# Kernel optimization log

Hardware: AMD Instinct MI355X
Metric: run time of the kernel (lower is better)

The kernel has to match this reference:

```python
import jax, jax.numpy as jnp
import numpy as np

N_NODES = 50000
N_EDGES = 600000
F_IN = 64
N_GRAPHS = 2000
OUT_DIM = 1
BN_EPS = 1e-5


def _bn(x, gamma, beta):
    # BatchNorm1d training-mode forward: biased batch stats over node/row dim
    m = jnp.mean(x, axis=0)
    v = jnp.var(x, axis=0)
    return (x - m) * jax.lax.rsqrt(v + BN_EPS) * gamma + beta


def _gcn(x, W, b, src, dst):
    # PyG GCNConv: h = x @ W; symmetric-normalized aggregation with self-loops; bias after agg
    n = x.shape[0]
    h = x @ W                                    # [N, C_out]
    ones = jnp.ones((src.shape[0],), h.dtype)
    deg = jax.ops.segment_sum(ones, dst, num_segments=n) + 1.0  # +1 self-loop
    dinv = jax.lax.rsqrt(deg)
    norm = (dinv[src] * dinv[dst])[:, None]      # [E, 1]
    agg = jax.ops.segment_sum(h[src] * norm, dst, num_segments=n)
    agg = agg + h * (1.0 / deg)[:, None]         # self-loop term: deg^{-1/2}*deg^{-1/2}
    return agg + b


def _pool_mean(x, batch, g):
    s = jax.ops.segment_sum(x, batch, num_segments=g)
    c = jax.ops.segment_sum(jnp.ones((x.shape[0],), x.dtype), batch, num_segments=g)
    return s / jnp.maximum(c, 1.0)[:, None]


def _forward(xc, xs, W1c, b1c, g1c, be1c, W2c, b2c, g2c, be2c,
             W1s, b1s, g1s, be1s, W2s, b2s, g2s, be2s,
             Wf1, bf1, gf1, bef1, Wf2, bf2,
             src_c, dst_c, src_s, dst_s, batch):
    hc = jax.nn.relu(_bn(_gcn(xc, W1c, b1c, src_c, dst_c), g1c, be1c))
    hc = jax.nn.relu(_bn(_gcn(hc, W2c, b2c, src_c, dst_c), g2c, be2c))
    hs = jax.nn.relu(_bn(_gcn(xs, W1s, b1s, src_s, dst_s), g1s, be1s))
    hs = jax.nn.relu(_bn(_gcn(hs, W2s, b2s, src_s, dst_s), g2s, be2s))
    pc = _pool_mean(hc, batch, N_GRAPHS)         # [G, 64]
    ps = _pool_mean(hs, batch, N_GRAPHS)         # [G, 64]
    h = jnp.concatenate([pc, ps], axis=1)        # [G, 128]
    h = jax.nn.relu(_bn(h @ Wf1 + bf1, gf1, bef1))  # dropout is identity in eval
    return h @ Wf2 + bf2                         # [G, OUT_DIM]


def setup_inputs() -> dict:
    key = jax.random.key(0)
    ks = jax.random.split(key, 16)

    def glorot(k, fan_in, fan_out):
        s = np.sqrt(2.0 / (fan_in + fan_out)).astype(np.float32)
        return jax.random.normal(k, (fan_in, fan_out), jnp.float32) * s

    inp = {
        'x_chromophore': jax.random.normal(ks[0], (N_NODES, F_IN), jnp.float32),
        'x_solvent': jax.random.normal(ks[1], (N_NODES, F_IN), jnp.float32),
        'edge_index_chromophore': jax.random.randint(ks[2], (2, N_EDGES), 0, N_NODES),
        'edge_index_solvent': jax.random.randint(ks[3], (2, N_EDGES), 0, N_NODES),
        'batch': jnp.sort(jax.random.randint(ks[4], (N_NODES,), 0, N_GRAPHS)),
        # chromophore branch params
        'W1c': glorot(ks[5], F_IN, 128), 'b1c': jnp.zeros((128,), jnp.float32),
        'g1c': jnp.ones((128,), jnp.float32), 'be1c': jnp.zeros((128,), jnp.float32),
        'W2c': glorot(ks[6], 128, 64), 'b2c': jnp.zeros((64,), jnp.float32),
        'g2c': jnp.ones((64,), jnp.float32), 'be2c': jnp.zeros((64,), jnp.float32),
        # solvent branch params
        'W1s': glorot(ks[7], F_IN, 128), 'b1s': jnp.zeros((128,), jnp.float32),
        'g1s': jnp.ones((128,), jnp.float32), 'be1s': jnp.zeros((128,), jnp.float32),
        'W2s': glorot(ks[8], 128, 64), 'b2s': jnp.zeros((64,), jnp.float32),
        'g2s': jnp.ones((64,), jnp.float32), 'be2s': jnp.zeros((64,), jnp.float32),
        # MLP head
        'Wf1': glorot(ks[9], 128, 64), 'bf1': jnp.zeros((64,), jnp.float32),
        'gf1': jnp.ones((64,), jnp.float32), 'bef1': jnp.zeros((64,), jnp.float32),
        'Wf2': glorot(ks[10], 64, OUT_DIM), 'bf2': jnp.zeros((OUT_DIM,), jnp.float32),
    }
    return inp


def reference(x_chromophore, x_solvent, edge_index_chromophore, edge_index_solvent, batch,
              W1c, b1c, g1c, be1c, W2c, b2c, g2c, be2c,
              W1s, b1s, g1s, be1s, W2s, b2s, g2s, be2s,
              Wf1, bf1, gf1, bef1, Wf2, bf2):
    src_c, dst_c = edge_index_chromophore[0], edge_index_chromophore[1]
    src_s, dst_s = edge_index_solvent[0], edge_index_solvent[1]
    return _forward(x_chromophore, x_solvent,
                    W1c, b1c, g1c, be1c, W2c, b2c, g2c, be2c,
                    W1s, b1s, g1s, be1s, W2s, b2s, g2s, be2s,
                    Wf1, bf1, gf1, bef1, Wf2, bf2,
                    src_c, dst_c, src_s, dst_s, batch)
```

## Files before the change

kernel.cpp:

```cpp
#include <hip/hip_runtime.h>
#include <hip/hip_bf16.h>
#include <cstdint>
#include <cstddef>

#define NN 50000
#define NE 600000
#define NG 2000
#define NBUCK 49
#define SLOTS 16
#define NCHUNK 3125

typedef __attribute__((ext_vector_type(8))) short bf8;
typedef __attribute__((ext_vector_type(4))) float f32x4;

__device__ __forceinline__ unsigned short f2bf(float f) {
    uint32_t u = __float_as_uint(f);
    uint32_t r = (u + 0x7FFFu + ((u >> 16) & 1u)) >> 16;
    return (unsigned short)r;
}
__device__ __forceinline__ float bf2f(unsigned short h) {
    return __uint_as_float(((uint32_t)h) << 16);
}
__device__ __forceinline__ float lo16(uint32_t v) { return __uint_as_float(v << 16); }
__device__ __forceinline__ float hi16(uint32_t v) { return __uint_as_float(v & 0xFFFF0000u); }

__global__ __launch_bounds__(256) void conv_bf16_kernel(const float* __restrict__ x0,
                                                        const float* __restrict__ x1,
                                                        unsigned short* __restrict__ out) {
    int b = blockIdx.y;
    const float* x = b ? x1 : x0;
    unsigned short* o = out + (size_t)b * NN * 64;
    int i = (blockIdx.x * 256 + threadIdx.x) * 4;
    if (i + 3 < NN * 64) {
        float4 v = *(const float4*)&x[i];
        ushort4 r = make_ushort4(f2bf(v.x), f2bf(v.y), f2bf(v.z), f2bf(v.w));
        *(ushort4*)&o[i] = r;
    }
}

template<int K, int N>
__global__ __launch_bounds__(256) void pack_w(const float* __restrict__ W0,
                                              const float* __restrict__ W1,
                                              unsigned short* __restrict__ out) {
    int b = blockIdx.y;
    const float* W = b ? W1 : W0;
    unsigned short* o = out + (size_t)b * K * N;
    int idx = blockIdx.x * 256 + threadIdx.x;
    const int total = (N / 16) * (K / 32) * 64;
    if (idx >= total) return;
    int l = idx & 63;
    int th = idx >> 6;
    int h = th % (K / 32);
    int t = th / (K / 32);
    int col = t * 16 + (l & 15);
    int k0 = h * 32 + (l >> 4) * 8;
    ushort4 lo = make_ushort4(f2bf(W[(k0 + 0) * N + col]), f2bf(W[(k0 + 1) * N + col]),
                              f2bf(W[(k0 + 2) * N + col]), f2bf(W[(k0 + 3) * N + col]));
    ushort4 hi = make_ushort4(f2bf(W[(k0 + 4) * N + col]), f2bf(W[(k0 + 5) * N + col]),
                              f2bf(W[(k0 + 6) * N + col]), f2bf(W[(k0 + 7) * N + col]));
    *(ushort4*)&o[idx * 8] = lo;
    *(ushort4*)&o[idx * 8 + 4] = hi;
}

__global__ __launch_bounds__(256) void bucket_hist(const int* __restrict__ d0,
                                                   const int* __restrict__ d1,
                                                   int* __restrict__ bucketCnt, int nE) {
    int b = blockIdx.y;
    const int* dst = b ? d1 : d0;
    __shared__ int h[NBUCK];
    for (int i = threadIdx.x; i < NBUCK; i += 256) h[i] = 0;
    __syncthreads();
    for (int e = blockIdx.x * 256 + threadIdx.x; e < nE; e += gridDim.x * 256)
        atomicAdd(&h[dst[e] >> 10], 1);
    __syncthreads();
    for (int i = threadIdx.x; i < NBUCK; i += 256)
        if (h[i]) atomicAdd(&bucketCnt[b * NBUCK + i], h[i]);
}

__global__ void bucket_scan(const int* __restrict__ bucketCnt,
                            int* __restrict__ bucketOff, int* __restrict__ bucketCur) {
    int b = threadIdx.x;
    if (b < 2) {
        int run = 0;
        for (int i = 0; i < NBUCK; ++i) {
            bucketOff[b * NBUCK + i] = run;
            bucketCur[b * NBUCK + i] = run;
            run += bucketCnt[b * NBUCK + i];
        }
    }
}

__global__ __launch_bounds__(256) void bucket_scatter(const int* __restrict__ s0,
                                                      const int* __restrict__ d0,
                                                      const int* __restrict__ s1,
                                                      const int* __restrict__ d1,
                                                      int* __restrict__ bucketCur,
                                                      uint32_t* __restrict__ bent, int nE) {
    int b = blockIdx.y;
    const int* src = b ? s1 : s0;
    const int* dst = b ? d1 : d0;
    __shared__ int cnt[NBUCK];
    __shared__ int base[NBUCK];
    const int tid = threadIdx.x;
    for (int i = tid; i < NBUCK; i += 256) cnt[i] = 0;
    __syncthreads();

    const int e0 = blockIdx.x * 2048 + tid;
    int bk[8], slot[8];
    uint32_t pay[8];
#pragma unroll
    for (int k = 0; k < 8; ++k) {
        int e = e0 + k * 256;
        if (e < nE) {
            int d = dst[e], s = src[e];
            bk[k] = d >> 10;
            pay[k] = ((uint32_t)(d & 1023) << 16) | (uint32_t)s;
            slot[k] = atomicAdd(&cnt[bk[k]], 1);
        } else bk[k] = -1;
    }
    __syncthreads();
    for (int i = tid; i < NBUCK; i += 256) {
        int c = cnt[i];
        base[i] = c ? atomicAdd(&bucketCur[b * NBUCK + i], c) : 0;
    }
    __syncthreads();
#pragma unroll
    for (int k = 0; k < 8; ++k)
        if (bk[k] >= 0)
            bent[(size_t)b * NE + base[bk[k]] + slot[k]] = pay[k];
}

__global__ __launch_bounds__(256) void csr_build(const uint32_t* __restrict__ bent,
                                                 const int* __restrict__ bucketOff,
                                                 const int* __restrict__ bucketCnt,
                                                 int* __restrict__ row_ptr,
                                                 float* __restrict__ dinv,
                                                 uint16_t* __restrict__ perm) {
    __shared__ int lcnt[1024];
    __shared__ int lcur[1024];
    __shared__ int sscan[256];
    const int bk = blockIdx.x;
    const int b = blockIdx.y;
    const int tid = threadIdx.x;
    const int ebase = bucketOff[b * NBUCK + bk];
    const int ecnt = bucketCnt[b * NBUCK + bk];
    const int node0 = bk << 10;
    const uint32_t* be = bent + (size_t)b * NE + ebase;
    int* rp = row_ptr + b * (NN + 1);
    float* dv = dinv + (size_t)b * NN;
    uint16_t* pm = perm + (size_t)b * NE + ebase;

    for (int i = tid; i < 1024; i += 256) lcnt[i] = 0;
    __syncthreads();
    for (int i = tid; i < ecnt; i += 256) atomicAdd(&lcnt[be[i] >> 16], 1);
    __syncthreads();

    int c[4], s = 0;
#pragma unroll
    for (int j = 0; j < 4; ++j) { c[j] = lcnt[tid * 4 + j]; s += c[j]; }
    sscan[tid] = s;
    __syncthreads();
    for (int off = 1; off < 256; off <<= 1) {
        int v = (tid >= off) ? sscan[tid - off] : 0;
        __syncthreads();
        sscan[tid] += v;
        __syncthreads();
    }
    int run = sscan[tid] - s;
#pragma unroll
    for (int j = 0; j < 4; ++j) {
        int nl = tid * 4 + j;
        int g = node0 + nl;
        if (g < NN) {
            rp[g] = ebase + run;
            lcur[nl] = run;
            dv[g] = rsqrtf((float)c[j] + 1.0f);
        }
        run += c[j];
    }
    if (bk == NBUCK - 1 && tid == 0) rp[NN] = ebase + ecnt;
    __syncthreads();

    for (int i = tid; i < ecnt; i += 256) {
        uint32_t en = be[i];
        int nl = en >> 16;
        int pos = atomicAdd(&lcur[nl], 1);
        pm[pos] = (uint16_t)(en & 0xFFFFu);
    }
}

__global__ __launch_bounds__(256) void weight_fill(const uint16_t* __restrict__ perm,
                                                   const float* __restrict__ dinv,
                                                   uint32_t* __restrict__ permw, int nE) {
    int b = blockIdx.y;
    const uint16_t* pm = perm + (size_t)b * NE;
    const float* dv = dinv + (size_t)b * NN;
    uint32_t* pw = permw + (size_t)b * NE;
    int i = (blockIdx.x * 256 + threadIdx.x) * 4;
    if (i + 3 < nE) {
        ushort4 s4 = *(const ushort4*)&pm[i];
        uint4 o;
        o.x = ((uint32_t)f2bf(dv[s4.x]) << 16) | (uint32_t)s4.x;
        o.y = ((uint32_t)f2bf(dv[s4.y]) << 16) | (uint32_t)s4.y;
        o.z = ((uint32_t)f2bf(dv[s4.z]) << 16) | (uint32_t)s4.z;
        o.w = ((uint32_t)f2bf(dv[s4.w]) << 16) | (uint32_t)s4.w;
        *(uint4*)&pw[i] = o;
    } else {
        for (; i < nE; ++i) {
            uint16_t s = pm[i];
            pw[i] = ((uint32_t)f2bf(dv[s]) << 16) | (uint32_t)s;
        }
    }
}

__global__ __launch_bounds__(256) void graph_ranges(const int* __restrict__ batch,
                                                    int* __restrict__ gstart,
                                                    int* __restrict__ gend, int n) {
    int i = blockIdx.x * 256 + threadIdx.x;
    if (i >= n) return;
    int g = batch[i];
    if (i == 0 || batch[i - 1] != g) gstart[g] = i;
    if (i == n - 1 || batch[i + 1] != g) gend[g] = i + 1;
}

__global__ __launch_bounds__(256) void gemm1_mfma(const unsigned short* __restrict__ Xbf,
                                                  const unsigned short* __restrict__ Wp,
                                                  unsigned short* __restrict__ Y) {
    const int b = blockIdx.y;
    const unsigned short* __restrict__ X = Xbf + (size_t)b * NN * 64;
    const unsigned short* __restrict__ W = Wp + (size_t)b * 64 * 128;
    unsigned short* __restrict__ Yb = Y + (size_t)b * NN * 128;
    const int tid = threadIdx.x;
    const int w = tid >> 6, lane = tid & 63;
    const int chunk = blockIdx.x * 4 + w;
    if (chunk >= NCHUNK) return;
    const int m = lane & 15, quad = lane >> 4;

    const int row = chunk * 16 + m;
    bf8 a0 = *(const bf8*)&X[(size_t)row * 64 + quad * 8];
    bf8 a1 = *(const bf8*)&X[(size_t)row * 64 + 32 + quad * 8];
    f32x4 acc[8];
#pragma unroll
    for (int t = 0; t < 8; ++t) acc[t] = (f32x4){0.f, 0.f, 0.f, 0.f};
#pragma unroll
    for (int t = 0; t < 8; ++t) {
        bf8 b0 = *(const bf8*)&W[((t * 2 + 0) * 64 + lane) * 8];
        bf8 b1 = *(const bf8*)&W[((t * 2 + 1) * 64 + lane) * 8];
        acc[t] = __builtin_amdgcn_mfma_f32_16x16x32_bf16(b0, a0, acc[t], 0, 0, 0);
        acc[t] = __builtin_amdgcn_mfma_f32_16x16x32_bf16(b1, a1, acc[t], 0, 0, 0);
    }
#pragma unroll
    for (int t = 0; t < 8; ++t) {
        uint32_t lo = (uint32_t)f2bf(acc[t][0]) | ((uint32_t)f2bf(acc[t][1]) << 16);
        uint32_t hi = (uint32_t)f2bf(acc[t][2]) | ((uint32_t)f2bf(acc[t][3]) << 16);
        *(uint2*)&Yb[(size_t)row * 128 + t * 16 + quad * 4] = make_uint2(lo, hi);
    }
}

__global__ __launch_bounds__(256) void stats128_bf16(const unsigned short* __restrict__ Y,
                                                     float* __restrict__ sums) {
    const int b = blockIdx.y;
    const unsigned short* __restrict__ Yb = Y + (size_t)b * NN * 128;
    const int g = threadIdx.x & 31;
    const int rs = threadIdx.x >> 5;
    float s0 = 0.f, s1 = 0.f, s2 = 0.f, s3 = 0.f;
    float q0 = 0.f, q1 = 0.f, q2 = 0.f, q3 = 0.f;
    for (int r = blockIdx.x * 8 + rs; r < NN; r += gridDim.x * 8) {
        uint2 v = *(const uint2*)&Yb[(size_t)r * 128 + g * 4];
        float x0 = lo16(v.x);
        float x1 = hi16(v.x);
        float x2 = lo16(v.y);
        float x3 = hi16(v.y);
        s0 += x0; s1 += x1; s2 += x2; s3 += x3;
        q0 = fmaf(x0, x0, q0); q1 = fmaf(x1, x1, q1);
        q2 = fmaf(x2, x2, q2); q3 = fmaf(x3, x3, q3);
    }
    __shared__ float ls[8][128], lq[8][128];
    *(float4*)&ls[rs][g * 4] = make_float4(s0, s1, s2, s3);
    *(float4*)&lq[rs][g * 4] = make_float4(q0, q1, q2, q3);
    __syncthreads();
    if (threadIdx.x < 128) {
        const int c = threadIdx.x;
        float S = 0.f, Q = 0.f;
#pragma unroll
        for (int k = 0; k < 8; ++k) { S += ls[k][c]; Q += lq[k][c]; }
        int slot = blockIdx.x & (SLOTS - 1);
        float* sb = sums + (size_t)(b * SLOTS + slot) * 256;
        atomicAdd(&sb[c], S);
        atomicAdd(&sb[128 + c], Q);
    }
}

__global__ __launch_bounds__(256) void gemm2_mfma(const unsigned short* __restrict__ H1,
                                                  const unsigned short* __restrict__ Wp,
                                                  const float* __restrict__ sums,
                                                  const float* __restrict__ g0,
                                                  const float* __restrict__ g1,
                                                  const float* __restrict__ be0,
                                                  const float* __restrict__ be1,
                                                  unsigned short* __restrict__ Y) {
    __shared__ float scLds[128], shLds[128];
    const int b = blockIdx.y;
    const unsigned short* __restrict__ X = H1 + (size_t)b * NN * 128;
    const unsigned short* __restrict__ W = Wp + (size_t)b * 128 * 64;
    unsigned short* __restrict__ Yb = Y + (size_t)b * NN * 64;
    const int tid = threadIdx.x;

    if (tid < 128) {
        float s = 0.f, s2 = 0.f;
#pragma unroll
        for (int k = 0; k < SLOTS; ++k) {
            const float* sb = sums + (size_t)(b * SLOTS + k) * 256;
            s += sb[tid];
            s2 += sb[128 + tid];
        }
        const float invN = 1.0f / (float)NN;
        float mean = s * invN;
        float var = s2 * invN - mean * mean;
        float gamma = b ? g1[tid] : g0[tid];
        float beta = b ? be1[tid] : be0[tid];
        float sc = gamma * rsqrtf(var + 1e-5f);
        scLds[tid] = sc;
        shLds[tid] = beta - mean * sc;
    }
    __syncthreads();

    const int w = tid >> 6, lane = tid & 63;
    const int chunk = blockIdx.x * 4 + w;
    if (chunk >= NCHUNK) return;
    const int m = lane & 15, quad = lane >> 4;
    const int row = chunk * 16 + m;

    f32x4 acc[4];
#pragma unroll
    for (int t = 0; t < 4; ++t) acc[t] = (f32x4){0.f, 0.f, 0.f, 0.f};
#pragma unroll
    for (int h = 0; h < 4; ++h) {
        const int k0 = h * 32 + quad * 8;
        bf8 araw = *(const bf8*)&X[(size_t)row * 128 + k0];
        float4 sc0 = *(const float4*)&scLds[k0];
        float4 sc1 = *(const float4*)&scLds[k0 + 4];
        float4 sh0 = *(const float4*)&shLds[k0];
        float4 sh1 = *(const float4*)&shLds[k0 + 4];
        float scv[8] = {sc0.x, sc0.y, sc0.z, sc0.w, sc1.x, sc1.y, sc1.z, sc1.w};
        float shv[8] = {sh0.x, sh0.y, sh0.z, sh0.w, sh1.x, sh1.y, sh1.z, sh1.w};
        bf8 af;
#pragma unroll
        for (int j = 0; j < 8; ++j) {
            float v = bf2f((unsigned short)araw[j]);
            v = fmaxf(fmaf(v, scv[j], shv[j]), 0.f);
            af[j] = (short)f2bf(v);
        }
#pragma unroll
        for (int t = 0; t < 4; ++t) {
            bf8 bf = *(const bf8*)&W[((t * 4 + h) * 64 + lane) * 8];
            acc[t] = __builtin_amdgcn_mfma_f32_16x16x32_bf16(bf, af, acc[t], 0, 0, 0);
        }
    }
#pragma unroll
    for (int t = 0; t < 4; ++t) {
        uint32_t lo = (uint32_t)f2bf(acc[t][0]) | ((uint32_t)f2bf(acc[t][1]) << 16);
        uint32_t hi = (uint32_t)f2bf(acc[t][2]) | ((uint32_t)f2bf(acc[t][3]) << 16);
        *(uint2*)&Yb[(size_t)row * 64 + t * 16 + quad * 4] = make_uint2(lo, hi);
    }
}

template<bool STATS>
__global__ __launch_bounds__(256) void agg2_kernel(const unsigned short* __restrict__ hall,
                                                   const int* __restrict__ row_ptr,
                                                   const uint32_t* __restrict__ permw,
                                                   const float* __restrict__ dinv,
                                                   unsigned short* __restrict__ out,
                                                   float* __restrict__ sums, int nNodes) {
    const int bid = blockIdx.x;
    const int xcd = bid & 7;
    const int b = xcd >> 2;
    const int j = (bid >> 3) * 4 + (xcd & 3);
    const unsigned short* __restrict__ h = hall + (size_t)b * NN * 64;
    const int* rp = row_ptr + b * (NN + 1);
    const uint32_t* pe = permw + (size_t)b * NE;
    const float* dv = dinv + (size_t)b * NN;
    unsigned short* ob = out + (size_t)b * nNodes * 64;

    const int w = threadIdx.x >> 6;
    const int wave = j * 4 + w;
    const int lane = threadIdx.x & 63;
    const int q = lane & 15;
    const int r = lane >> 4;
    float f0 = 0.f, f1 = 0.f, f2 = 0.f, f3 = 0.f;
    const bool active = wave < nNodes;
    if (active) {
        const int d = wave;
        const float di = dv[d];
        const int p0 = rp[d], p1 = rp[d + 1];
        float a0 = 0.f, a1 = 0.f, a2 = 0.f, a3 = 0.f;
        for (int p = p0; p < p1; p += 16) {
            uint32_t en[4];
#pragma unroll
            for (int k = 0; k < 4; ++k) {
                int e = p + k * 4 + r;
                bool vld = e < p1;
                en[k] = pe[vld ? e : p0];
                if (!vld) en[k] &= 0xFFFFu;
            }
#pragma unroll
            for (int k = 0; k < 4; ++k) {
                const int idx = (int)(en[k] & 0xFFFFu);
                const float wk = __uint_as_float(en[k] & 0xFFFF0000u);
                const uint2 hv = *(const uint2*)&h[(size_t)idx * 64 + q * 4];
                a0 = fmaf(wk, lo16(hv.x), a0);
                a1 = fmaf(wk, hi16(hv.x), a1);
                a2 = fmaf(wk, lo16(hv.y), a2);
                a3 = fmaf(wk, hi16(hv.y), a3);
            }
        }
        a0 += __shfl_xor(a0, 16, 64); a0 += __shfl_xor(a0, 32, 64);
        a1 += __shfl_xor(a1, 16, 64); a1 += __shfl_xor(a1, 32, 64);
        a2 += __shfl_xor(a2, 16, 64); a2 += __shfl_xor(a2, 32, 64);
        a3 += __shfl_xor(a3, 16, 64); a3 += __shfl_xor(a3, 32, 64);
        const uint2 sv = *(const uint2*)&h[(size_t)d * 64 + q * 4];
        f0 = di * fmaf(di, lo16(sv.x), a0);
        f1 = di * fmaf(di, hi16(sv.x), a1);
        f2 = di * fmaf(di, lo16(sv.y), a2);
        f3 = di * fmaf(di, hi16(sv.y), a3);
        if (r == 0) {
            uint32_t o0 = (uint32_t)f2bf(f0) | ((uint32_t)f2bf(f1) << 16);
            uint32_t o1 = (uint32_t)f2bf(f2) | ((uint32_t)f2bf(f3) << 16);
            *(uint2*)&ob[(size_t)d * 64 + q * 4] = make_uint2(o0, o1);
        }
    }
    if constexpr (STATS) {
        __shared__ float ls[256], ls2[256];
        if (lane < 16) {
            *(float4*)&ls[w * 64 + q * 4]  = make_float4(f0, f1, f2, f3);
            *(float4*)&ls2[w * 64 + q * 4] = make_float4(f0 * f0, f1 * f1, f2 * f2, f3 * f3);
        }
        __syncthreads();
        if (threadIdx.x < 64) {
            const int t = threadIdx.x;
            float s  = ls[t]  + ls[t + 64]  + ls[t + 128]  + ls[t + 192];
            float s2 = ls2[t] + ls2[t + 64] + ls2[t + 128] + ls2[t + 192];
            int slot = j & (SLOTS - 1);
            float* sb = sums + ((size_t)(b * SLOTS + slot) * 2) * 64;
            atomicAdd(&sb[t], s);
            atomicAdd(&sb[64 + t], s2);
        }
    }
}

__global__ __launch_bounds__(128) void pool_head_kernel(const unsigned short* __restrict__ x,
                                                        const float* __restrict__ sums,
                                                        const float* __restrict__ g0,
                                                        const float* __restrict__ g1,
                                                        const float* __restrict__ be0,
                                                        const float* __restrict__ be1,
                                                        const int* __restrict__ gstart,
                                                        const int* __restrict__ gend,
                                                        const float* __restrict__ Wf1,
                                                        float* __restrict__ T) {
    __shared__ float row[128];
    const int g = blockIdx.x;
    const int c = threadIdx.x;
    const int b = c >> 6;
    const int ch = c & 63;
    float s0 = 0.f, s20 = 0.f;
#pragma unroll
    for (int k = 0; k < SLOTS; ++k) {
        const float* sb = sums + ((size_t)(b * SLOTS + k) * 2) * 64;
        s0 += sb[ch];
        s20 += sb[64 + ch];
    }
    const float invN = 1.0f / (float)NN;
    float mean = s0 * invN;
    float var = s20 * invN - mean * mean;
    float gamma = b ? g1[ch] : g0[ch];
    float beta = b ? be1[ch] : be0[ch];
    float sc = gamma * rsqrtf(var + 1e-5f);
    float sh = beta - mean * sc;

    const unsigned short* xb = x + (size_t)b * NN * 64;
    const int start = gstart[g];
    const int end = gend[g];
    float s = 0.f;
    for (int r = start; r < end; ++r)
        s += fmaxf(fmaf(bf2f(xb[(size_t)r * 64 + ch]), sc, sh), 0.f);
    float cf = (float)(end - start);
    row[c] = s / fmaxf(cf, 1.f);
    __syncthreads();

    if (c < 64) {
        float acc = 0.f;
#pragma unroll 8
        for (int k = 0; k < 128; ++k) acc = fmaf(row[k], Wf1[k * 64 + c], acc);
        T[(size_t)g * 64 + c] = acc;
    }
}

template<int C>
__global__ __launch_bounds__(256) void bn_stats_kernel(const float* __restrict__ x, int n,
                                                       float* __restrict__ sums) {
    constexpr int RP = 256 / C;
    __shared__ float ls[256], ls2[256];
    int c = threadIdx.x % C;
    int sub = threadIdx.x / C;
    float s = 0.f, s2 = 0.f;
    for (int r = blockIdx.x * RP + sub; r < n; r += gridDim.x * RP) {
        float v = x[(size_t)r * C + c];
        s += v; s2 += v * v;
    }
    ls[threadIdx.x] = s; ls2[threadIdx.x] = s2;
    __syncthreads();
    if (sub == 0) {
#pragma unroll
        for (int k = 1; k < RP; ++k) { s += ls[k * C + c]; s2 += ls2[k * C + c]; }
        atomicAdd(&sums[c], s);
        atomicAdd(&sums[C + c], s2);
    }
}

__global__ __launch_bounds__(64) void head_final_kernel(const float* __restrict__ T,
                                                        const float* __restrict__ hsums,
                                                        const float* __restrict__ gf1,
                                                        const float* __restrict__ bef1,
                                                        const float* __restrict__ Wf2,
                                                        const float* __restrict__ bf2,
                                                        float* __restrict__ out) {
    int g = blockIdx.x;
    int c = threadIdx.x;
    const float invG = 1.0f / (float)NG;
    float mean = hsums[c] * invG;
    float var = hsums[64 + c] * invG - mean * mean;
    float sc = gf1[c] * rsqrtf(var + 1e-5f);
    float sh = bef1[c] - mean * sc;
    float v = fmaxf(fmaf(T[(size_t)g * 64 + c], sc, sh), 0.f) * Wf2[c];
#pragma unroll
    for (int off = 32; off > 0; off >>= 1) v += __shfl_down(v, off, 64);
    if (c == 0) out[g] = v + bf2[0];
}


static inline size_t alignup(size_t x) { return (x + 255) & ~(size_t)255; }

extern "C" void kernel_launch(void* const* d_in, const int* in_sizes, int n_in,
                              void* d_out, int out_size, void* d_ws, size_t ws_size,
                              hipStream_t stream) {
    const float* xc  = (const float*)d_in[0];
    const float* xs  = (const float*)d_in[1];
    const int*   eic = (const int*)d_in[2];
    const int*   eis = (const int*)d_in[3];
    const int*   batch = (const int*)d_in[4];
    const float* W1c = (const float*)d_in[5];
    const float* g1c = (const float*)d_in[7];
    const float* be1c = (const float*)d_in[8];
    const float* W2c = (const float*)d_in[9];
    const float* g2c = (const float*)d_in[11];
    const float* be2c = (const float*)d_in[12];
    const float* W1s = (const float*)d_in[13];
    const float* g1s = (const float*)d_in[15];
    const float* be1s = (const float*)d_in[16];
    const float* W2s = (const float*)d_in[17];
    const float* g2s = (const float*)d_in[19];
    const float* be2s = (const float*)d_in[20];
    const float* Wf1 = (const float*)d_in[21];
    const float* gf1 = (const float*)d_in[23];
    const float* bef1 = (const float*)d_in[24];
    const float* Wf2 = (const float*)d_in[25];
    const float* bf2 = (const float*)d_in[26];
    float* out = (float*)d_out;

    char* ws = (char*)d_ws;
    size_t off = 0;
    auto alloc = [&](size_t bytes) { char* p = ws + off; off += alignup(bytes); return p; };

    int*      bucketCnt = (int*)alloc(2 * NBUCK * 4);
    int*      bucketOff = (int*)alloc(2 * NBUCK * 4);
    int*      bucketCur = (int*)alloc(2 * NBUCK * 4);
    uint32_t* bent      = (uint32_t*)alloc((size_t)2 * NE * 4);
    uint16_t* perm      = (uint16_t*)alloc(((size_t)2 * NE + 64) * 2);
    int*      row_ptr   = (int*)alloc(2 * (NN + 1) * 4);
    float*    dinv      = (float*)alloc((size_t)2 * NN * 4);
    int*      gbound    = (int*)alloc((size_t)2 * NG * 4);
    unsigned short* xbf   = (unsigned short*)alloc((size_t)2 * NN * 64 * 2);
    unsigned short* aggbf = (unsigned short*)alloc((size_t)2 * NN * 64 * 2);
    unsigned short* h1bf  = (unsigned short*)alloc((size_t)2 * NN * 128 * 2);
    unsigned short* h2bf  = (unsigned short*)alloc((size_t)2 * NN * 64 * 2);
    unsigned short* Wp1   = (unsigned short*)alloc((size_t)2 * 64 * 128 * 2);
    unsigned short* Wp2   = (unsigned short*)alloc((size_t)2 * 128 * 64 * 2);
    float*    sums1     = (float*)alloc(((size_t)2 * SLOTS * 256 + (size_t)2 * SLOTS * 128 + 128) * 4);
    float*    sums2     = sums1 + (size_t)2 * SLOTS * 256;
    float*    hsums     = sums2 + (size_t)2 * SLOTS * 128;
    float*    T         = (float*)alloc((size_t)NG * 64 * 4);
    int*      gstart    = gbound;
    int*      gend      = gbound + NG;

    const size_t statBytes = ((size_t)2 * SLOTS * 256 + (size_t)2 * SLOTS * 128 + 128) * 4;
    const int gemmBlocks = (NCHUNK + 3) / 4;
    const int aggBlocks = 25000;

    conv_bf16_kernel<<<dim3((NN * 64 / 4 + 255) / 256, 2), 256, 0, stream>>>(xc, xs, xbf);
    pack_w<64, 128><<<dim3(4, 2), 256, 0, stream>>>(W1c, W1s, Wp1);
    pack_w<128, 64><<<dim3(4, 2), 256, 0, stream>>>(W2c, W2s, Wp2);
    hipMemsetAsync(sums1, 0, statBytes, stream);
    hipMemsetAsync(gbound, 0, 2 * NG * 4, stream);
    graph_ranges<<<(NN + 255) / 256, 256, 0, stream>>>(batch, gstart, gend, NN);

    hipMemsetAsync(bucketCnt, 0, 2 * NBUCK * 4, stream);
    bucket_hist<<<dim3(64, 2), 256, 0, stream>>>(eic + NE, eis + NE, bucketCnt, NE);
    bucket_scan<<<1, 64, 0, stream>>>(bucketCnt, bucketOff, bucketCur);
    bucket_scatter<<<dim3((NE + 2047) / 2048, 2), 256, 0, stream>>>(
        eic, eic + NE, eis, eis + NE, bucketCur, bent, NE);
    csr_build<<<dim3(NBUCK, 2), 256, 0, stream>>>(bent, bucketOff, bucketCnt,
                                                  row_ptr, dinv, perm);
    weight_fill<<<dim3((NE / 4 + 255) / 256, 2), 256, 0, stream>>>(perm, dinv, bent, NE);

    agg2_kernel<false><<<aggBlocks, 256, 0, stream>>>(
        xbf, row_ptr, bent, dinv, aggbf, nullptr, NN);
    gemm1_mfma<<<dim3(gemmBlocks, 2), 256, 0, stream>>>(aggbf, Wp1, h1bf);
    stats128_bf16<<<dim3(256, 2), 256, 0, stream>>>(h1bf, sums1);

    gemm2_mfma<<<dim3(gemmBlocks, 2), 256, 0, stream>>>(h1bf, Wp2, sums1,
                                                        g1c, g1s, be1c, be1s, h2bf);
    agg2_kernel<true><<<aggBlocks, 256, 0, stream>>>(
        h2bf, row_ptr, bent, dinv, aggbf, sums2, NN);

    pool_head_kernel<<<NG, 128, 0, stream>>>(aggbf, sums2, g2c, g2s, be2c, be2s,
                                             gstart, gend, Wf1, T);

    bn_stats_kernel<64><<<32, 256, 0, stream>>>(T, NG, hsums);
    head_final_kernel<<<NG, 64, 0, stream>>>(T, hsums, gf1, bef1, Wf2, bf2, out);
}
```

Before: 346.2 us.

## Pack per-node degree, dinv and first edges into 128-byte records for aggregation

Adds a rec_fill kernel that writes one 32-word record per node holding the edge count, dinv, the row offset and up to 28 packed edge entries. The aggregation kernel then loads the record with a single coalesced read and broadcasts the entries by shuffle, replacing separate row_ptr, dinv and edge-list loads. This removes dependent pointer-chasing latency in both aggregation passes. In exchange it adds an extra kernel and about 25 MB of record writes, and nodes with more than 28 edges still take the old loop.

```diff
diff --git a/kernel.cpp b/kernel.cpp
--- a/kernel.cpp
+++ b/kernel.cpp
@@ -9,6 +9,8 @@
 #define NBUCK 49
 #define SLOTS 16
 #define NCHUNK 3125
+#define RECW 32
+#define RECE 28
 
 typedef __attribute__((ext_vector_type(8))) short bf8;
 typedef __attribute__((ext_vector_type(4))) float f32x4;
@@ -213,6 +215,35 @@
     }
 }
 
+__global__ __launch_bounds__(256) void rec_fill(const int* __restrict__ row_ptr,
+                                                const float* __restrict__ dinv,
+                                                const uint32_t* __restrict__ permw,
+                                                uint32_t* __restrict__ recb) {
+    const int b = blockIdx.y;
+    const int tid = threadIdx.x;
+    const int node = blockIdx.x * 16 + (tid >> 4);
+    const int sub = tid & 15;
+    if (node >= NN) return;
+    const int* rp = row_ptr + b * (NN + 1);
+    const uint32_t* pe = permw + (size_t)b * NE;
+    const int p0 = rp[node], p1 = rp[node + 1];
+    const int cnt = p1 - p0;
+    const int cmin = cnt < RECE ? cnt : RECE;
+    uint2 o;
+    if (sub == 0) {
+        o.x = (uint32_t)cnt;
+        o.y = __float_as_uint(dinv[(size_t)b * NN + node]);
+    } else if (sub == 1) {
+        o.x = (uint32_t)p0;
+        o.y = 0u;
+    } else {
+        int j0 = sub * 2 - 4;
+        o.x = (j0 < cmin) ? pe[p0 + j0] : 0u;
+        o.y = (j0 + 1 < cmin) ? pe[p0 + j0 + 1] : 0u;
+    }
+    *(uint2*)&recb[((size_t)b * NN + node) * RECW + sub * 2] = o;
+}
+
 __global__ __launch_bounds__(256) void graph_ranges(const int* __restrict__ batch,
                                                     int* __restrict__ gstart,
                                                     int* __restrict__ gend, int n) {
@@ -366,10 +397,9 @@
 }
 
 template<bool STATS>
-__global__ __launch_bounds__(256) void agg2_kernel(const unsigned short* __restrict__ hall,
-                                                   const int* __restrict__ row_ptr,
+__global__ __launch_bounds__(256) void agg4_kernel(const unsigned short* __restrict__ hall,
+                                                   const uint32_t* __restrict__ recb,
                                                    const uint32_t* __restrict__ permw,
-                                                   const float* __restrict__ dinv,
                                                    unsigned short* __restrict__ out,
                                                    float* __restrict__ sums, int nNodes) {
     const int bid = blockIdx.x;
@@ -377,41 +407,57 @@
     const int b = xcd >> 2;
     const int j = (bid >> 3) * 4 + (xcd & 3);
     const unsigned short* __restrict__ h = hall + (size_t)b * NN * 64;
-    const int* rp = row_ptr + b * (NN + 1);
+    const uint32_t* __restrict__ rec = recb + (size_t)b * NN * RECW;
     const uint32_t* pe = permw + (size_t)b * NE;
-    const float* dv = dinv + (size_t)b * NN;
     unsigned short* ob = out + (size_t)b * nNodes * 64;
 
     const int w = threadIdx.x >> 6;
-    const int wave = j * 4 + w;
+    const int d = j * 4 + w;
     const int lane = threadIdx.x & 63;
     const int q = lane & 15;
     const int r = lane >> 4;
     float f0 = 0.f, f1 = 0.f, f2 = 0.f, f3 = 0.f;
-    const bool active = wave < nNodes;
+    const bool active = d < nNodes;
     if (active) {
-        const int d = wave;
-        const float di = dv[d];
-        const int p0 = rp[d], p1 = rp[d + 1];
+        const uint32_t rv = rec[(size_t)d * RECW + (lane & 31)];
+        const int cnt = (int)__shfl(rv, 0, 64);
+        const float di = __uint_as_float(__shfl(rv, 1, 64));
+        const int cmin = cnt < RECE ? cnt : RECE;
         float a0 = 0.f, a1 = 0.f, a2 = 0.f, a3 = 0.f;
-        for (int p = p0; p < p1; p += 16) {
-            uint32_t en[4];
-#pragma unroll
-            for (int k = 0; k < 4; ++k) {
-                int e = p + k * 4 + r;
-                bool vld = e < p1;
-                en[k] = pe[vld ? e : p0];
-                if (!vld) en[k] &= 0xFFFFu;
-            }
-#pragma unroll
-            for (int k = 0; k < 4; ++k) {
-                const int idx = (int)(en[k] & 0xFFFFu);
-                const float wk = __uint_as_float(en[k] & 0xFFFF0000u);
-                const uint2 hv = *(const uint2*)&h[(size_t)idx * 64 + q * 4];
-                a0 = fmaf(wk, lo16(hv.x), a0);
-                a1 = fmaf(wk, hi16(hv.x), a1);
-                a2 = fmaf(wk, lo16(hv.y), a2);
-                a3 = fmaf(wk, hi16(hv.y), a3);
+#pragma unroll
+        for (int k = 0; k < 7; ++k) {
+            if (k * 4 >= cmin) break;
+            const uint32_t en = __shfl(rv, 4 + k * 4 + r, 64);
+            const int idx = (int)(en & 0xFFFFu);
+            const float wk = __uint_as_float(en & 0xFFFF0000u);
+            const uint2 hv = *(const uint2*)&h[(size_t)idx * 64 + q * 4];
+            a0 = fmaf(wk, lo16(hv.x), a0);
+            a1 = fmaf(wk, hi16(hv.x), a1);
+            a2 = fmaf(wk, lo16(hv.y), a2);
+            a3 = fmaf(wk, hi16(hv.y), a3);
+        }
+        if (cnt > RECE) {
+            const int p0 = (int)__shfl(rv, 2, 64);
+            const int p1 = p0 + cnt;
+            for (int p = p0 + RECE; p < p1; p += 16) {
+                uint32_t en[4];
+#pragma unroll
+                for (int k = 0; k < 4; ++k) {
+                    int e = p + k * 4 + r;
+                    bool vld = e < p1;
+                    en[k] = pe[vld ? e : p0];
+                    if (!vld) en[k] &= 0xFFFFu;
+                }
+#pragma unroll
+                for (int k = 0; k < 4; ++k) {
+                    const int idx = (int)(en[k] & 0xFFFFu);
+                    const float wk = __uint_as_float(en[k] & 0xFFFF0000u);
+                    const uint2 hv = *(const uint2*)&h[(size_t)idx * 64 + q * 4];
+                    a0 = fmaf(wk, lo16(hv.x), a0);
+                    a1 = fmaf(wk, hi16(hv.x), a1);
+                    a2 = fmaf(wk, lo16(hv.y), a2);
+                    a3 = fmaf(wk, hi16(hv.y), a3);
+                }
             }
         }
         a0 += __shfl_xor(a0, 16, 64); a0 += __shfl_xor(a0, 32, 64);
@@ -579,6 +625,7 @@
     uint16_t* perm      = (uint16_t*)alloc(((size_t)2 * NE + 64) * 2);
     int*      row_ptr   = (int*)alloc(2 * (NN + 1) * 4);
     float*    dinv      = (float*)alloc((size_t)2 * NN * 4);
+    uint32_t* recb      = (uint32_t*)alloc((size_t)2 * NN * RECW * 4);
     int*      gbound    = (int*)alloc((size_t)2 * NG * 4);
     unsigned short* xbf   = (unsigned short*)alloc((size_t)2 * NN * 64 * 2);
     unsigned short* aggbf = (unsigned short*)alloc((size_t)2 * NN * 64 * 2);
@@ -612,16 +659,17 @@
     csr_build<<<dim3(NBUCK, 2), 256, 0, stream>>>(bent, bucketOff, bucketCnt,
                                                   row_ptr, dinv, perm);
     weight_fill<<<dim3((NE / 4 + 255) / 256, 2), 256, 0, stream>>>(perm, dinv, bent, NE);
-
-    agg2_kernel<false><<<aggBlocks, 256, 0, stream>>>(
-        xbf, row_ptr, bent, dinv, aggbf, nullptr, NN);
+    rec_fill<<<dim3((NN + 15) / 16, 2), 256, 0, stream>>>(row_ptr, dinv, bent, recb);
+
+    agg4_kernel<false><<<aggBlocks, 256, 0, stream>>>(
+        xbf, recb, bent, aggbf, nullptr, NN);
     gemm1_mfma<<<dim3(gemmBlocks, 2), 256, 0, stream>>>(aggbf, Wp1, h1bf);
     stats128_bf16<<<dim3(256, 2), 256, 0, stream>>>(h1bf, sums1);
 
     gemm2_mfma<<<dim3(gemmBlocks, 2), 256, 0, stream>>>(h1bf, Wp2, sums1,
                                                         g1c, g1s, be1c, be1s, h2bf);
-    agg2_kernel<true><<<aggBlocks, 256, 0, stream>>>(
-        h2bf, row_ptr, bent, dinv, aggbf, sums2, NN);
+    agg4_kernel<true><<<aggBlocks, 256, 0, stream>>>(
+        h2bf, recb, bent, aggbf, sums2, NN);
 
     pool_head_kernel<<<NG, 128, 0, stream>>>(aggbf, sums2, g2c, g2s, be2c, be2s,
                                              gstart, gend, Wf1, T);
```

Result: slower. 354.2 us (+2.3%).
